# Kernel optimization log

Hardware: AMD Instinct MI355X
Metric: run time of the kernel (lower is better)

Reference implementation:

```python
import math
import jax, jax.numpy as jnp
import numpy as np

B, N, D_INNER, D_STATE = 2, 4096, 384, 16


def setup_inputs() -> dict:
    key = jax.random.key(0)
    ks = jax.random.split(key, 6)
    dt_init = math.log(math.exp(0.1) - 1.0)
    x = jax.random.normal(ks[0], (B, N, D_INNER), jnp.float32)
    W_ds = jax.random.uniform(ks[1], (D_INNER, D_INNER), jnp.float32, -1e-4, 1e-4)
    b_ds = jnp.full((D_INNER,), dt_init, jnp.float32)
    W_dd = jax.random.uniform(ks[2], (D_INNER, D_INNER), jnp.float32, -1e-4, 1e-4)
    b_dd = jnp.full((D_INNER,), dt_init, jnp.float32)
    W_B = jax.random.normal(ks[3], (D_INNER, D_STATE), jnp.float32) * 0.05
    W_C = jax.random.normal(ks[4], (D_INNER, D_STATE), jnp.float32) * 0.05
    D_param = jnp.ones((D_INNER,), jnp.float32)
    A_log = jnp.tile(jnp.log(jnp.arange(1, D_STATE + 1, dtype=jnp.float32))[None, :], (D_INNER, 1))
    diff_raw = jnp.zeros((1, D_INNER, 1, 1), jnp.float32)
    return {"x": x, "W_ds": W_ds, "b_ds": b_ds, "W_dd": W_dd, "b_dd": b_dd,
            "W_B": W_B, "W_C": W_C, "D_param": D_param, "A_log": A_log,
            "diff_raw": diff_raw, "K_steps": 3}


def _laplacian(h_2d, d):
    # hard-coded heat-equation stencil, depthwise 3x3 conv, padding=1
    lap = jnp.array([[0.0, 1.0, 0.0], [1.0, -4.0, 1.0], [0.0, 1.0, 0.0]], jnp.float32)
    kernel = jnp.tile(lap[None, None], (d, 1, 1, 1))  # (D,1,3,3) OIHW
    return jax.lax.conv_general_dilated(
        h_2d, kernel, window_strides=(1, 1), padding=((1, 1), (1, 1)),
        feature_group_count=d, dimension_numbers=("NCHW", "OIHW", "NCHW"))


def reference(x, W_ds, b_ds, W_dd, b_dd, W_B, W_C, D_param, A_log, diff_raw, K_steps):
    Bv, Nn, Dd = x.shape
    Hh = Ww = int(math.isqrt(Nn))
    dt = 1.0 / K_steps
    A_mat = -jax.nn.softplus(A_log)                                 # (D,S)
    delta_self = jnp.minimum(jax.nn.softplus(x @ W_ds + b_ds), 0.15)  # (B,N,D)
    delta_diff = jnp.minimum(jax.nn.softplus(x @ W_dd + b_dd), 0.15)  # (B,N,D)
    B_mat = x @ W_B                                                  # (B,N,S)
    C_mat = x @ W_C                                                  # (B,N,S)
    mamba_input = x[..., None] * B_mat[:, :, None, :]                # (B,N,D,S)
    D_phys = jax.nn.sigmoid(diff_raw) * 0.5                          # (1,D,1,1)

    h = mamba_input
    for _ in range(K_steps):
        h_spatial = h.sum(axis=-1)                                   # (B,N,D)
        h_2d = jnp.transpose(h_spatial, (0, 2, 1)).reshape(Bv, Dd, Hh, Ww)
        lap_h = _laplacian(h_2d, Dd)
        diffused = (D_phys * lap_h).reshape(Bv, Dd, Nn)
        diffused = jnp.transpose(diffused, (0, 2, 1))                # (B,N,D)
        mamba_decay = h * A_mat[None, None]                          # (B,N,D,S)
        force_1 = delta_self[..., None] * (mamba_decay + mamba_input)
        force_2 = delta_diff[..., None] * diffused[..., None]
        h = h + dt * (force_1 + force_2)

    y = jnp.einsum("bnds,bns->bnd", h, C_mat)
    return y + x * D_param
```

## Files before the change

kernel.cpp:

```cpp
#include <hip/hip_runtime.h>
#include <math.h>

#define Bv 2
#define Nn 4096
#define Dd 384
#define HH 64
#define NROWS (Bv * Nn)
#define TOT ((size_t)NROWS * Dd)
#define NPAD 896
static const float DT = 1.0f / 3.0f;

typedef short bf16x8 __attribute__((ext_vector_type(8)));
typedef float f32x4 __attribute__((ext_vector_type(4)));
typedef float f4 __attribute__((ext_vector_type(4)));

__device__ __forceinline__ short f2bf(float f) {
    unsigned u = __builtin_bit_cast(unsigned, f);
    u += 0x7FFF + ((u >> 16) & 1);
    return (short)(u >> 16);
}

__device__ __forceinline__ float fast_softplus(float z) {
    return __logf(1.0f + __expf(z));
}

__device__ __forceinline__ void gl2lds16(const void* g, void* l) {
    __builtin_amdgcn_global_load_lds(
        (const __attribute__((address_space(1))) unsigned int*)g,
        (__attribute__((address_space(3))) unsigned int*)l, 16, 0, 0);
}

__global__ __launch_bounds__(256) void prep_all(
    const float* __restrict__ x, short* __restrict__ xb, float* __restrict__ xT,
    const float* __restrict__ W_ds, const float* __restrict__ W_dd,
    const float* __restrict__ W_B, const float* __restrict__ W_C,
    short* __restrict__ WbT)
{
    __shared__ float T[64][65];
    int b = blockIdx.x, t = threadIdx.x;
    if (b < 768) {
        int rt = b / 6, ct = b - rt * 6;
        int r0 = rt * 64, c0 = ct * 64;
#pragma unroll
        for (int l = 0; l < 4; ++l) {
            int idx = t + l * 256;
            int rr = idx >> 4, cc = (idx & 15) * 4;
            f4 v = *(const f4*)(x + (size_t)(r0 + rr) * Dd + c0 + cc);
            T[rr][cc + 0] = v.x; T[rr][cc + 1] = v.y;
            T[rr][cc + 2] = v.z; T[rr][cc + 3] = v.w;
            short4 o;
            o.x = f2bf(v.x); o.y = f2bf(v.y); o.z = f2bf(v.z); o.w = f2bf(v.w);
            *(short4*)(xb + (size_t)(r0 + rr) * Dd + c0 + cc) = o;
        }
        __syncthreads();
#pragma unroll
        for (int l = 0; l < 4; ++l) {
            int idx = t + l * 256;
            int rr = idx >> 4, cc = (idx & 15) * 4;
            f4 v;
            v.x = T[cc + 0][rr]; v.y = T[cc + 1][rr];
            v.z = T[cc + 2][rr]; v.w = T[cc + 3][rr];
            *(f4*)(xT + (size_t)(c0 + rr) * NROWS + r0 + cc) = v;
        }
    } else {
        int n = b - 768;
        for (int k = t; k < 384; k += 256) {
            float v;
            if (n < 384)      v = W_ds[(size_t)k * 384 + n];
            else if (n < 768) v = W_dd[(size_t)k * 384 + (n - 384)];
            else if (n < 784) v = W_B[k * 16 + (n - 768)];
            else if (n < 800) v = W_C[k * 16 + (n - 784)];
            else              v = 0.f;
            WbT[(size_t)n * 384 + k] = f2bf(v);
        }
    }
}

__global__ __launch_bounds__(256) void gemm_t(
    const short* __restrict__ xb, const short* __restrict__ WbT,
    const float* __restrict__ b_ds, const float* __restrict__ b_dd,
    const float* __restrict__ diff_raw,
    float* __restrict__ gT, float* __restrict__ wT,
    float* __restrict__ BmT, float* __restrict__ CmT)
{
    __shared__ short As[2][64][32];
    __shared__ short Bs[2][128][32];

    const int n0 = blockIdx.x * 128;
    const int m0 = blockIdx.y * 64;
    const int t = threadIdx.x;
    const int w = t >> 6;
    const int lane = t & 63;
    const int ln15 = lane & 15, quad = lane >> 4;
    const int wr = (w >> 1) * 32;
    const int wc = (w & 1) * 64;

    const int srow = lane >> 2;
    const int sq   = (lane & 3) * 8;
    const short* agp  = WbT + (size_t)(m0 + w * 16 + srow) * 384 + sq;
    const short* bgp0 = xb  + (size_t)(n0 + w * 32 + srow) * 384 + sq;
    const short* bgp1 = xb  + (size_t)(n0 + w * 32 + 16 + srow) * 384 + sq;

    f32x4 acc[2][4];
#pragma unroll
    for (int i = 0; i < 2; ++i)
#pragma unroll
        for (int j = 0; j < 4; ++j) acc[i][j] = (f32x4)0.f;

    for (int it = 0; it < 6; ++it) {
        const int kk = it * 64;
#pragma unroll
        for (int s = 0; s < 2; ++s) {
            const int ks = kk + s * 32;
            gl2lds16(agp + ks, &As[s][w * 16][0]);
            gl2lds16(bgp0 + ks, &Bs[s][w * 32][0]);
            gl2lds16(bgp1 + ks, &Bs[s][w * 32 + 16][0]);
        }
        __syncthreads();

        bf16x8 af[2][2], bfr[4][2];
#pragma unroll
        for (int s = 0; s < 2; ++s) {
#pragma unroll
            for (int ti = 0; ti < 2; ++ti)
                af[ti][s] = *(const bf16x8*)&As[s][wr + ti * 16 + ln15][quad * 8];
#pragma unroll
            for (int tj = 0; tj < 4; ++tj)
                bfr[tj][s] = *(const bf16x8*)&Bs[s][wc + tj * 16 + ln15][quad * 8];
        }
#pragma unroll
        for (int s = 0; s < 2; ++s)
#pragma unroll
            for (int ti = 0; ti < 2; ++ti)
#pragma unroll
                for (int tj = 0; tj < 4; ++tj)
                    acc[ti][tj] = __builtin_amdgcn_mfma_f32_16x16x32_bf16(
                        af[ti][s], bfr[tj][s], acc[ti][tj], 0, 0, 0);
        __syncthreads();
    }

#pragma unroll
    for (int ti = 0; ti < 2; ++ti) {
#pragma unroll
        for (int tj = 0; tj < 4; ++tj) {
            int rg = n0 + wc + tj * 16 + ln15;
#pragma unroll
            for (int r = 0; r < 4; ++r) {
                int dg = m0 + wr + ti * 16 + quad * 4 + r;
                float v = acc[ti][tj][r];
                if (dg < 384) {
                    float dlt = fminf(fast_softplus(v + b_ds[dg]), 0.15f);
                    gT[(size_t)dg * NROWS + rg] = DT * dlt;
                } else if (dg < 768) {
                    int d = dg - 384;
                    float dlt = fminf(fast_softplus(v + b_dd[d]), 0.15f);
                    float dph = 0.5f / (1.0f + __expf(-diff_raw[d]));
                    wT[(size_t)d * NROWS + rg] = DT * dlt * dph;
                } else if (dg < 784) {
                    BmT[(size_t)(dg - 768) * NROWS + rg] = v;
                } else if (dg < 800) {
                    CmT[(size_t)(dg - 784) * NROWS + rg] = v;
                }
            }
        }
    }
}

__global__ __launch_bounds__(256) void rowmom_kernel(
    const float* __restrict__ BmT, const float* __restrict__ CmT,
    const float* __restrict__ A_log, float* __restrict__ AsumP,
    float* __restrict__ rmT)
{
    __shared__ float a1s[16], a2s[16], a3s[16];
    int t = threadIdx.x;
    if (t < 16) {
        float a = -log1pf(expf(A_log[t]));
        a1s[t] = a; a2s[t] = a * a; a3s[t] = a * a * a;
    }
    __syncthreads();
    if (blockIdx.x == 0 && t == 0) {
        float s = 0.f;
        for (int i = 0; i < 16; ++i) s += a1s[i];
        AsumP[0] = s;
    }
    int row = blockIdx.x * 256 + t;
    float P0 = 0, P1 = 0, P2 = 0, Q0 = 0, Q1 = 0, Q2 = 0, Q3 = 0, V0 = 0, V1 = 0, V2 = 0;
#pragma unroll
    for (int s = 0; s < 16; ++s) {
        float Bvv = BmT[(size_t)s * NROWS + row], Cv = CmT[(size_t)s * NROWS + row];
        float a1 = a1s[s], a2 = a2s[s], a3 = a3s[s];
        P0 += Bvv; P1 += a1 * Bvv; P2 += a2 * Bvv;
        float bc = Bvv * Cv;
        Q0 += bc; Q1 += a1 * bc; Q2 += a2 * bc; Q3 += a3 * bc;
        V0 += Cv; V1 += a1 * Cv; V2 += a2 * Cv;
    }
    rmT[0 * NROWS + row] = P0; rmT[1 * NROWS + row] = P1; rmT[2 * NROWS + row] = P2;
    rmT[3 * NROWS + row] = Q0; rmT[4 * NROWS + row] = Q1; rmT[5 * NROWS + row] = Q2;
    rmT[6 * NROWS + row] = Q3;
    rmT[7 * NROWS + row] = V0; rmT[8 * NROWS + row] = V1; rmT[9 * NROWS + row] = V2;
}

__global__ __launch_bounds__(256) void fused_steps(
    const float* __restrict__ xT, const float* __restrict__ gT,
    const float* __restrict__ wT, const float* __restrict__ rmT,
    const float* __restrict__ AsumP, const float* __restrict__ D_param,
    float* __restrict__ yT)
{
    __shared__ float Sa[4096], Sb[4096];
    const int d = blockIdx.x, b = blockIdx.y;
    const int t = threadIdx.x;
    const size_t co = (size_t)d * NROWS + b * Nn;
    const float* xc = xT + co;
    const float* gc = gT + co;
    const float* wc = wT + co;
    const float* rP0 = rmT + 0 * NROWS + b * Nn;
    const float* rP1 = rmT + 1 * NROWS + b * Nn;
    const float* rP2 = rmT + 2 * NROWS + b * Nn;
    const float Asum = AsumP[0];
    const float Dp = D_param[d];

    float xv[16], gv[16], wv[16], p0v[16], c0[16], c1[16], sown[16];

#pragma unroll
    for (int e = 0; e < 16; ++e) {
        int n = e * 256 + t;
        xv[e] = xc[n]; gv[e] = gc[n]; wv[e] = wc[n];
        p0v[e] = rP0[n];
        sown[e] = xv[e] * p0v[e];
        Sa[n] = sown[e];
    }
    __syncthreads();

#pragma unroll
    for (int e = 0; e < 16; ++e) {
        int n = e * 256 + t, i = n >> 6, j = n & 63;
        float l = -4.0f * sown[e];
        if (i > 0)  l += Sa[n - 64];
        if (i < 63) l += Sa[n + 64];
        if (j > 0)  l += Sa[n - 1];
        if (j < 63) l += Sa[n + 1];
        c0[e] = wv[e] * l;
        float T0 = sown[e], T1 = xv[e] * rP1[n];
        sown[e] = (1.0f + gv[e]) * T0 + gv[e] * T1 + 16.0f * c0[e];
        Sb[n] = sown[e];
    }
    __syncthreads();

#pragma unroll
    for (int e = 0; e < 16; ++e) {
        int n = e * 256 + t, i = n >> 6, j = n & 63;
        float l = -4.0f * sown[e];
        if (i > 0)  l += Sb[n - 64];
        if (i < 63) l += Sb[n + 64];
        if (j > 0)  l += Sb[n - 1];
        if (j < 63) l += Sb[n + 1];
        c1[e] = wv[e] * l;
        float T0 = xv[e] * p0v[e], T1 = xv[e] * rP1[n], T2 = xv[e] * rP2[n];
        float g = gv[e], g2 = g * g;
        sown[e] = (1.0f + 2.0f * g) * T0 + (2.0f * g + g2) * T1 + g2 * T2
                + c0[e] * (16.0f + g * Asum) + 16.0f * c1[e];
        Sa[n] = sown[e];
    }
    __syncthreads();

#pragma unroll
    for (int e = 0; e < 16; ++e) {
        int n = e * 256 + t, i = n >> 6, j = n & 63;
        float l = -4.0f * sown[e];
        if (i > 0)  l += Sa[n - 64];
        if (i < 63) l += Sa[n + 64];
        if (j > 0)  l += Sa[n - 1];
        if (j < 63) l += Sa[n + 1];
        float c2 = wv[e] * l;
        float q0 = rmT[3 * NROWS + b * Nn + n], q1 = rmT[4 * NROWS + b * Nn + n];
        float q2 = rmT[5 * NROWS + b * Nn + n], q3 = rmT[6 * NROWS + b * Nn + n];
        float v0 = rmT[7 * NROWS + b * Nn + n], v1 = rmT[8 * NROWS + b * Nn + n];
        float v2 = rmT[9 * NROWS + b * Nn + n];
        float g = gv[e], g2 = g * g, g3 = g2 * g;
        yT[co + n] = xv[e] * (q0 * (1.0f + 3.0f * g) + q1 * (3.0f * g + 3.0f * g2)
                            + q2 * (3.0f * g2 + g3) + q3 * g3 + Dp)
                   + c0[e] * (v0 + 2.0f * g * v1 + g2 * v2)
                   + c1[e] * (v0 + g * v1)
                   + c2 * v0;
    }
}

__global__ __launch_bounds__(256) void transpose_y(
    const float* __restrict__ yT, float* __restrict__ y)
{
    __shared__ float T[64][65];
    int r0 = blockIdx.x * 64, d0 = blockIdx.y * 64;
    int t = threadIdx.x;
#pragma unroll
    for (int l = 0; l < 4; ++l) {
        int idx = t + l * 256;
        int rr = idx >> 4, cc = (idx & 15) * 4;
        f4 v = *(const f4*)(yT + (size_t)(d0 + rr) * NROWS + r0 + cc);
        T[rr][cc + 0] = v.x; T[rr][cc + 1] = v.y;
        T[rr][cc + 2] = v.z; T[rr][cc + 3] = v.w;
    }
    __syncthreads();
#pragma unroll
    for (int l = 0; l < 4; ++l) {
        int idx = t + l * 256;
        int rr = idx >> 4, cc = (idx & 15) * 4;
        f4 v;
        v.x = T[cc + 0][rr]; v.y = T[cc + 1][rr];
        v.z = T[cc + 2][rr]; v.w = T[cc + 3][rr];
        *(f4*)(y + (size_t)(r0 + rr) * Dd + d0 + cc) = v;
    }
}

extern "C" void kernel_launch(void* const* d_in, const int* in_sizes, int n_in,
                              void* d_out, int out_size, void* d_ws, size_t ws_size,
                              hipStream_t stream) {
    const float* x        = (const float*)d_in[0];
    const float* W_ds     = (const float*)d_in[1];
    const float* b_ds     = (const float*)d_in[2];
    const float* W_dd     = (const float*)d_in[3];
    const float* b_dd     = (const float*)d_in[4];
    const float* W_B      = (const float*)d_in[5];
    const float* W_C      = (const float*)d_in[6];
    const float* D_param  = (const float*)d_in[7];
    const float* A_log    = (const float*)d_in[8];
    const float* diff_raw = (const float*)d_in[9];

    float* wsf = (float*)d_ws;
    const size_t M = TOT;
    float* gT    = wsf;
    float* wT    = wsf + 1 * M;
    float* xT    = wsf + 2 * M;
    float* yT    = wsf + 3 * M;
    float* BmT   = wsf + 4 * M;
    float* CmT   = BmT + (size_t)16 * NROWS;
    float* rmT   = CmT + (size_t)16 * NROWS;
    float* AsumP = rmT + (size_t)10 * NROWS;
    short* xb    = (short*)(AsumP + 16);
    short* WbT   = xb + M;

    float* y = (float*)d_out;

    prep_all<<<768 + NPAD, 256, 0, stream>>>(x, xb, xT, W_ds, W_dd, W_B, W_C, WbT);
    gemm_t<<<dim3(NROWS / 128, NPAD / 64), 256, 0, stream>>>(
        xb, WbT, b_ds, b_dd, diff_raw, gT, wT, BmT, CmT);
    rowmom_kernel<<<NROWS / 256, 256, 0, stream>>>(BmT, CmT, A_log, AsumP, rmT);
    fused_steps<<<dim3(Dd, Bv), 256, 0, stream>>>(xT, gT, wT, rmT, AsumP, D_param, yT);
    transpose_y<<<dim3(128, 6), 256, 0, stream>>>(yT, y);
}
```

Measured before the change: 144.9 us.

## Store intermediates in bf16, fuse row moments into GEMM, trim padded GEMM tiles

Switches the transposed x copy, the g/w coefficient buffers and the transposed output to bf16, which halves the memory traffic through the intermediate buffers between kernels. The B/C row-moment computation moves into the GEMM epilogue: the last M-tile block stages B and C through shared memory and writes the moments, so the separate rowmom kernel launch and the BmT/CmT buffers are gone. The GEMM grid shrinks from 14 to 13 M-tiles so the all-zero padding tile is skipped. In exchange the coefficients, input and output lose precision to bf16 rounding, which could exceed the accuracy tolerance.

After: 154.9 us. 1.07x slower.

```diff
diff --git a/kernel.cpp b/kernel.cpp
--- a/kernel.cpp
+++ b/kernel.cpp
@@ -4,7 +4,6 @@
 #define Bv 2
 #define Nn 4096
 #define Dd 384
-#define HH 64
 #define NROWS (Bv * Nn)
 #define TOT ((size_t)NROWS * Dd)
 #define NPAD 896
@@ -19,6 +18,9 @@
     u += 0x7FFF + ((u >> 16) & 1);
     return (short)(u >> 16);
 }
+__device__ __forceinline__ float bf2f(unsigned short u) {
+    return __builtin_bit_cast(float, (unsigned)u << 16);
+}
 
 __device__ __forceinline__ float fast_softplus(float z) {
     return __logf(1.0f + __expf(z));
@@ -31,7 +33,7 @@
 }
 
 __global__ __launch_bounds__(256) void prep_all(
-    const float* __restrict__ x, short* __restrict__ xb, float* __restrict__ xT,
+    const float* __restrict__ x, short* __restrict__ xb, unsigned short* __restrict__ xT,
     const float* __restrict__ W_ds, const float* __restrict__ W_dd,
     const float* __restrict__ W_B, const float* __restrict__ W_C,
     short* __restrict__ WbT)
@@ -57,10 +59,10 @@
         for (int l = 0; l < 4; ++l) {
             int idx = t + l * 256;
             int rr = idx >> 4, cc = (idx & 15) * 4;
-            f4 v;
-            v.x = T[cc + 0][rr]; v.y = T[cc + 1][rr];
-            v.z = T[cc + 2][rr]; v.w = T[cc + 3][rr];
-            *(f4*)(xT + (size_t)(c0 + rr) * NROWS + r0 + cc) = v;
+            short4 o;
+            o.x = f2bf(T[cc + 0][rr]); o.y = f2bf(T[cc + 1][rr]);
+            o.z = f2bf(T[cc + 2][rr]); o.w = f2bf(T[cc + 3][rr]);
+            *(short4*)(xT + (size_t)(c0 + rr) * NROWS + r0 + cc) = o;
         }
     } else {
         int n = b - 768;
@@ -79,12 +81,15 @@
 __global__ __launch_bounds__(256) void gemm_t(
     const short* __restrict__ xb, const short* __restrict__ WbT,
     const float* __restrict__ b_ds, const float* __restrict__ b_dd,
-    const float* __restrict__ diff_raw,
-    float* __restrict__ gT, float* __restrict__ wT,
-    float* __restrict__ BmT, float* __restrict__ CmT)
+    const float* __restrict__ diff_raw, const float* __restrict__ A_log,
+    unsigned short* __restrict__ gT, unsigned short* __restrict__ wT,
+    float* __restrict__ rmT, float* __restrict__ AsumP)
 {
-    __shared__ short As[2][64][32];
-    __shared__ short Bs[2][128][32];
+    union SmemU {
+        struct { short A[2][64][32]; short B[2][128][32]; } g;
+        struct { float fb[32][132]; float a1[16], a2[16], a3[16]; } r;
+    };
+    __shared__ SmemU sm;
 
     const int n0 = blockIdx.x * 128;
     const int m0 = blockIdx.y * 64;
@@ -112,9 +117,9 @@
 #pragma unroll
         for (int s = 0; s < 2; ++s) {
             const int ks = kk + s * 32;
-            gl2lds16(agp + ks, &As[s][w * 16][0]);
-            gl2lds16(bgp0 + ks, &Bs[s][w * 32][0]);
-            gl2lds16(bgp1 + ks, &Bs[s][w * 32 + 16][0]);
+            gl2lds16(agp + ks, &sm.g.A[s][w * 16][0]);
+            gl2lds16(bgp0 + ks, &sm.g.B[s][w * 32][0]);
+            gl2lds16(bgp1 + ks, &sm.g.B[s][w * 32 + 16][0]);
         }
         __syncthreads();
 
@@ -123,10 +128,10 @@
         for (int s = 0; s < 2; ++s) {
 #pragma unroll
             for (int ti = 0; ti < 2; ++ti)
-                af[ti][s] = *(const bf16x8*)&As[s][wr + ti * 16 + ln15][quad * 8];
+                af[ti][s] = *(const bf16x8*)&sm.g.A[s][wr + ti * 16 + ln15][quad * 8];
 #pragma unroll
             for (int tj = 0; tj < 4; ++tj)
-                bfr[tj][s] = *(const bf16x8*)&Bs[s][wc + tj * 16 + ln15][quad * 8];
+                bfr[tj][s] = *(const bf16x8*)&sm.g.B[s][wc + tj * 16 + ln15][quad * 8];
         }
 #pragma unroll
         for (int s = 0; s < 2; ++s)
@@ -137,6 +142,12 @@
                     acc[ti][tj] = __builtin_amdgcn_mfma_f32_16x16x32_bf16(
                         af[ti][s], bfr[tj][s], acc[ti][tj], 0, 0, 0);
         __syncthreads();
+    }
+
+    const bool mom = (blockIdx.y == 12);
+    if (mom && t < 16) {
+        float a = -log1pf(expf(A_log[t]));
+        sm.r.a1[t] = a; sm.r.a2[t] = a * a; sm.r.a3[t] = a * a * a;
     }
 
 #pragma unroll
@@ -150,69 +161,60 @@
                 float v = acc[ti][tj][r];
                 if (dg < 384) {
                     float dlt = fminf(fast_softplus(v + b_ds[dg]), 0.15f);
-                    gT[(size_t)dg * NROWS + rg] = DT * dlt;
+                    gT[(size_t)dg * NROWS + rg] = (unsigned short)f2bf(DT * dlt);
                 } else if (dg < 768) {
                     int d = dg - 384;
                     float dlt = fminf(fast_softplus(v + b_dd[d]), 0.15f);
                     float dph = 0.5f / (1.0f + __expf(-diff_raw[d]));
-                    wT[(size_t)d * NROWS + rg] = DT * dlt * dph;
-                } else if (dg < 784) {
-                    BmT[(size_t)(dg - 768) * NROWS + rg] = v;
+                    wT[(size_t)d * NROWS + rg] = (unsigned short)f2bf(DT * dlt * dph);
                 } else if (dg < 800) {
-                    CmT[(size_t)(dg - 784) * NROWS + rg] = v;
+                    sm.r.fb[dg - 768][rg - n0] = v;
                 }
             }
         }
     }
-}
-
-__global__ __launch_bounds__(256) void rowmom_kernel(
-    const float* __restrict__ BmT, const float* __restrict__ CmT,
-    const float* __restrict__ A_log, float* __restrict__ AsumP,
-    float* __restrict__ rmT)
-{
-    __shared__ float a1s[16], a2s[16], a3s[16];
-    int t = threadIdx.x;
-    if (t < 16) {
-        float a = -log1pf(expf(A_log[t]));
-        a1s[t] = a; a2s[t] = a * a; a3s[t] = a * a * a;
-    }
-    __syncthreads();
-    if (blockIdx.x == 0 && t == 0) {
-        float s = 0.f;
-        for (int i = 0; i < 16; ++i) s += a1s[i];
-        AsumP[0] = s;
-    }
-    int row = blockIdx.x * 256 + t;
-    float P0 = 0, P1 = 0, P2 = 0, Q0 = 0, Q1 = 0, Q2 = 0, Q3 = 0, V0 = 0, V1 = 0, V2 = 0;
-#pragma unroll
-    for (int s = 0; s < 16; ++s) {
-        float Bvv = BmT[(size_t)s * NROWS + row], Cv = CmT[(size_t)s * NROWS + row];
-        float a1 = a1s[s], a2 = a2s[s], a3 = a3s[s];
-        P0 += Bvv; P1 += a1 * Bvv; P2 += a2 * Bvv;
-        float bc = Bvv * Cv;
-        Q0 += bc; Q1 += a1 * bc; Q2 += a2 * bc; Q3 += a3 * bc;
-        V0 += Cv; V1 += a1 * Cv; V2 += a2 * Cv;
-    }
-    rmT[0 * NROWS + row] = P0; rmT[1 * NROWS + row] = P1; rmT[2 * NROWS + row] = P2;
-    rmT[3 * NROWS + row] = Q0; rmT[4 * NROWS + row] = Q1; rmT[5 * NROWS + row] = Q2;
-    rmT[6 * NROWS + row] = Q3;
-    rmT[7 * NROWS + row] = V0; rmT[8 * NROWS + row] = V1; rmT[9 * NROWS + row] = V2;
+
+    if (mom) {
+        __syncthreads();
+        if (t < 128) {
+            int row = n0 + t;
+            float P0 = 0, P1 = 0, P2 = 0, Q0 = 0, Q1 = 0, Q2 = 0, Q3 = 0,
+                  V0 = 0, V1 = 0, V2 = 0;
+#pragma unroll
+            for (int s = 0; s < 16; ++s) {
+                float Bvv = sm.r.fb[s][t], Cv = sm.r.fb[16 + s][t];
+                float a1 = sm.r.a1[s], a2 = sm.r.a2[s], a3 = sm.r.a3[s];
+                P0 += Bvv; P1 += a1 * Bvv; P2 += a2 * Bvv;
+                float bc = Bvv * Cv;
+                Q0 += bc; Q1 += a1 * bc; Q2 += a2 * bc; Q3 += a3 * bc;
+                V0 += Cv; V1 += a1 * Cv; V2 += a2 * Cv;
+            }
+            rmT[0 * NROWS + row] = P0; rmT[1 * NROWS + row] = P1; rmT[2 * NROWS + row] = P2;
+            rmT[3 * NROWS + row] = Q0; rmT[4 * NROWS + row] = Q1; rmT[5 * NROWS + row] = Q2;
+            rmT[6 * NROWS + row] = Q3;
+            rmT[7 * NROWS + row] = V0; rmT[8 * NROWS + row] = V1; rmT[9 * NROWS + row] = V2;
+        }
+        if (blockIdx.x == 0 && t == 0) {
+            float s = 0.f;
+            for (int i = 0; i < 16; ++i) s += sm.r.a1[i];
+            AsumP[0] = s;
+        }
+    }
 }
 
 __global__ __launch_bounds__(256) void fused_steps(
-    const float* __restrict__ xT, const float* __restrict__ gT,
-    const float* __restrict__ wT, const float* __restrict__ rmT,
+    const unsigned short* __restrict__ xT, const unsigned short* __restrict__ gT,
+    const unsigned short* __restrict__ wT, const float* __restrict__ rmT,
     const float* __restrict__ AsumP, const float* __restrict__ D_param,
-    float* __restrict__ yT)
+    unsigned short* __restrict__ yT)
 {
     __shared__ float Sa[4096], Sb[4096];
     const int d = blockIdx.x, b = blockIdx.y;
     const int t = threadIdx.x;
     const size_t co = (size_t)d * NROWS + b * Nn;
-    const float* xc = xT + co;
-    const float* gc = gT + co;
-    const float* wc = wT + co;
+    const unsigned short* xc = xT + co;
+    const unsigned short* gc = gT + co;
+    const unsigned short* wc = wT + co;
     const float* rP0 = rmT + 0 * NROWS + b * Nn;
     const float* rP1 = rmT + 1 * NROWS + b * Nn;
     const float* rP2 = rmT + 2 * NROWS + b * Nn;
@@ -224,7 +226,7 @@
 #pragma unroll
     for (int e = 0; e < 16; ++e) {
         int n = e * 256 + t;
-        xv[e] = xc[n]; gv[e] = gc[n]; wv[e] = wc[n];
+        xv[e] = bf2f(xc[n]); gv[e] = bf2f(gc[n]); wv[e] = bf2f(wc[n]);
         p0v[e] = rP0[n];
         sown[e] = xv[e] * p0v[e];
         Sa[n] = sown[e];
@@ -277,16 +279,17 @@
         float v0 = rmT[7 * NROWS + b * Nn + n], v1 = rmT[8 * NROWS + b * Nn + n];
         float v2 = rmT[9 * NROWS + b * Nn + n];
         float g = gv[e], g2 = g * g, g3 = g2 * g;
-        yT[co + n] = xv[e] * (q0 * (1.0f + 3.0f * g) + q1 * (3.0f * g + 3.0f * g2)
-                            + q2 * (3.0f * g2 + g3) + q3 * g3 + Dp)
-                   + c0[e] * (v0 + 2.0f * g * v1 + g2 * v2)
-                   + c1[e] * (v0 + g * v1)
-                   + c2 * v0;
+        float yv = xv[e] * (q0 * (1.0f + 3.0f * g) + q1 * (3.0f * g + 3.0f * g2)
+                          + q2 * (3.0f * g2 + g3) + q3 * g3 + Dp)
+                 + c0[e] * (v0 + 2.0f * g * v1 + g2 * v2)
+                 + c1[e] * (v0 + g * v1)
+                 + c2 * v0;
+        yT[co + n] = (unsigned short)f2bf(yv);
     }
 }
 
 __global__ __launch_bounds__(256) void transpose_y(
-    const float* __restrict__ yT, float* __restrict__ y)
+    const unsigned short* __restrict__ yT, float* __restrict__ y)
 {
     __shared__ float T[64][65];
     int r0 = blockIdx.x * 64, d0 = blockIdx.y * 64;
@@ -295,9 +298,9 @@
     for (int l = 0; l < 4; ++l) {
         int idx = t + l * 256;
         int rr = idx >> 4, cc = (idx & 15) * 4;
-        f4 v = *(const f4*)(yT + (size_t)(d0 + rr) * NROWS + r0 + cc);
-        T[rr][cc + 0] = v.x; T[rr][cc + 1] = v.y;
-        T[rr][cc + 2] = v.z; T[rr][cc + 3] = v.w;
+        ushort4 v = *(const ushort4*)(yT + (size_t)(d0 + rr) * NROWS + r0 + cc);
+        T[rr][cc + 0] = bf2f(v.x); T[rr][cc + 1] = bf2f(v.y);
+        T[rr][cc + 2] = bf2f(v.z); T[rr][cc + 3] = bf2f(v.w);
     }
     __syncthreads();
 #pragma unroll
@@ -325,25 +328,21 @@
     const float* A_log    = (const float*)d_in[8];
     const float* diff_raw = (const float*)d_in[9];
 
-    float* wsf = (float*)d_ws;
     const size_t M = TOT;
-    float* gT    = wsf;
-    float* wT    = wsf + 1 * M;
-    float* xT    = wsf + 2 * M;
-    float* yT    = wsf + 3 * M;
-    float* BmT   = wsf + 4 * M;
-    float* CmT   = BmT + (size_t)16 * NROWS;
-    float* rmT   = CmT + (size_t)16 * NROWS;
+    unsigned short* gT = (unsigned short*)d_ws;
+    unsigned short* wT = gT + M;
+    unsigned short* xT = wT + M;
+    unsigned short* yT = xT + M;
+    short* xb  = (short*)(yT + M);
+    short* WbT = xb + M;
+    float* rmT   = (float*)(WbT + (size_t)NPAD * 384);
     float* AsumP = rmT + (size_t)10 * NROWS;
-    short* xb    = (short*)(AsumP + 16);
-    short* WbT   = xb + M;
 
     float* y = (float*)d_out;
 
-    prep_all<<<768 + NPAD, 256, 0, stream>>>(x, xb, xT, W_ds, W_dd, W_B, W_C, WbT);
-    gemm_t<<<dim3(NROWS / 128, NPAD / 64), 256, 0, stream>>>(
-        xb, WbT, b_ds, b_dd, diff_raw, gT, wT, BmT, CmT);
-    rowmom_kernel<<<NROWS / 256, 256, 0, stream>>>(BmT, CmT, A_log, AsumP, rmT);
+    prep_all<<<768 + 832, 256, 0, stream>>>(x, xb, xT, W_ds, W_dd, W_B, W_C, WbT);
+    gemm_t<<<dim3(NROWS / 128, 13), 256, 0, stream>>>(
+        xb, WbT, b_ds, b_dd, diff_raw, A_log, gT, wT, rmT, AsumP);
     fused_steps<<<dim3(Dd, Bv), 256, 0, stream>>>(xT, gT, wT, rmT, AsumP, D_param, yT);
     transpose_y<<<dim3(128, 6), 256, 0, stream>>>(yT, y);
 }
```
